# Kernel tuning notes

Hardware: AMD Instinct MI355X
Metric: run time of the kernel (lower is better)

## Reference

```python
import jax, jax.numpy as jnp
import numpy as np

H = 768      # hidden_size
NH = 12      # num_attention_heads
DH = H // NH # attention_head_size
FF = 3072    # intermediate_size
E = 4        # n_expert
B, S = 8, 512
EPS = 1e-12


def _layernorm(x, g, b):
    mu = jnp.mean(x, axis=-1, keepdims=True)
    var = jnp.var(x, axis=-1, keepdims=True)
    return (x - mu) * jax.lax.rsqrt(var + EPS) * g + b


def _expert_linear(x, W, b, expert_idx):
    # W: [E, in, out], b: [E, out]; gather per-sample expert weights, then batched GEMM.
    # Mathematically identical to running every expert then slicing (single_select_fwd).
    Wg = W[expert_idx]            # [B, in, out]
    bg = b[expert_idx]            # [B, out]
    return jnp.einsum('bsi,bio->bso', x, Wg) + bg[:, None, :]


def setup_inputs() -> dict:
    key = jax.random.key(0)
    ks = jax.random.split(key, 16)
    sc = 0.02
    inp = {
        'hidden_states': jax.random.normal(ks[0], (B, S, H), jnp.float32),
        'expert_idx': jax.random.randint(ks[1], (B,), 0, E, jnp.int64) if jax.config.read('jax_enable_x64') else jax.random.randint(ks[1], (B,), 0, E).astype(jnp.int32),
        'attention_mask': jnp.zeros((B, 1, 1, S), jnp.float32),
        'Wq': sc * jax.random.normal(ks[2], (E, H, H), jnp.float32),
        'bq': jnp.zeros((E, H), jnp.float32),
        'Wk': sc * jax.random.normal(ks[3], (E, H, H), jnp.float32),
        'bk': jnp.zeros((E, H), jnp.float32),
        'Wv': sc * jax.random.normal(ks[4], (E, H, H), jnp.float32),
        'bv': jnp.zeros((E, H), jnp.float32),
        'Wo': sc * jax.random.normal(ks[5], (E, H, H), jnp.float32),
        'bo': jnp.zeros((E, H), jnp.float32),
        'ln1_g': jnp.ones((H,), jnp.float32),
        'ln1_b': jnp.zeros((H,), jnp.float32),
        'Wi': sc * jax.random.normal(ks[6], (E, H, FF), jnp.float32),
        'bi': jnp.zeros((E, FF), jnp.float32),
        'Wout': sc * jax.random.normal(ks[7], (E, FF, H), jnp.float32),
        'bout': jnp.zeros((E, H), jnp.float32),
        'ln2_g': jnp.ones((H,), jnp.float32),
        'ln2_b': jnp.zeros((H,), jnp.float32),
    }
    return inp


def reference(hidden_states, expert_idx, attention_mask, Wq, bq, Wk, bk, Wv, bv,
              Wo, bo, ln1_g, ln1_b, Wi, bi, Wout, bout, ln2_g, ln2_b):
    b, s, h = hidden_states.shape
    # --- MoE self-attention (per-sample expert QKV) ---
    q = _expert_linear(hidden_states, Wq, bq, expert_idx).reshape(b, s, NH, DH).transpose(0, 2, 1, 3)
    k = _expert_linear(hidden_states, Wk, bk, expert_idx).reshape(b, s, NH, DH).transpose(0, 2, 1, 3)
    v = _expert_linear(hidden_states, Wv, bv, expert_idx).reshape(b, s, NH, DH).transpose(0, 2, 1, 3)
    scores = jnp.einsum('bhqd,bhkd->bhqk', q, k) / np.sqrt(DH).astype(np.float32)
    scores = scores + attention_mask
    probs = jax.nn.softmax(scores, axis=-1)
    ctx = jnp.einsum('bhqk,bhkd->bhqd', probs, v).transpose(0, 2, 1, 3).reshape(b, s, h)
    # --- MoE self-output: dense + residual + LN ---
    attn_out = _expert_linear(ctx, Wo, bo, expert_idx)
    x = _layernorm(attn_out + hidden_states, ln1_g, ln1_b)
    # --- MoE FFN: intermediate (GELU) + output + residual + LN ---
    hmid = jax.nn.gelu(_expert_linear(x, Wi, bi, expert_idx), approximate=False)
    ffn = _expert_linear(hmid, Wout, bout, expert_idx)
    return _layernorm(ffn + x, ln2_g, ln2_b)
```

## Files before the change

### kernel.cpp

```cpp
#include <hip/hip_runtime.h>
#include <cstdint>
#include <cstddef>

constexpr int CB  = 8;
constexpr int CS  = 512;
constexpr int CH  = 768;
constexpr int CNH = 12;
constexpr int CDH = 64;
constexpr int CFF = 3072;
constexpr int CE  = 4;
constexpr int C3H = 3 * CH;

using f32x4  = __attribute__((ext_vector_type(4))) float;
using bf16x8 = __attribute__((ext_vector_type(8))) short;

__device__ __forceinline__ short f2bf(float x) {
  union { float f; uint32_t u; } v; v.f = x;
  return (short)((v.u + 0x7fffu + ((v.u >> 16) & 1u)) >> 16);
}

__device__ __forceinline__ void gload_lds16(const void* g, void* l) {
  __builtin_amdgcn_global_load_lds((const __attribute__((address_space(1))) void*)g,
                                   (__attribute__((address_space(3))) void*)l,
                                   16, 0, 0);
}

#define VMCNT(n)  asm volatile("s_waitcnt vmcnt(" #n ")" ::: "memory")
#define SCHEDB()  __builtin_amdgcn_sched_barrier(0)

__global__ void cvt_bf16_kernel(const float* __restrict__ in, short* __restrict__ out, int n4) {
  int i = blockIdx.x * blockDim.x + threadIdx.x;
  if (i < n4) {
    float4 v = ((const float4*)in)[i];
    short4 o;
    o.x = f2bf(v.x); o.y = f2bf(v.y); o.z = f2bf(v.z); o.w = f2bf(v.w);
    ((short4*)out)[i] = o;
  }
}

__device__ __forceinline__ bool expert_used(const int* __restrict__ eidx, int e) {
  bool u = false;
#pragma unroll
  for (int s = 0; s < CB; ++s) u |= (eidx[s] == e);
  return u;
}

__device__ __forceinline__ void tpose_body(const float* __restrict__ Wb,
                                           short* __restrict__ Wtb, int K, int N) {
  __shared__ __align__(16) short Ts[64 * 68];
  const int n0 = blockIdx.x * 64, k0 = blockIdx.y * 64;
  const int t  = threadIdx.x;
  const int tn = t & 15, tk = t >> 4;
#pragma unroll
  for (int p = 0; p < 4; ++p) {
    int k = k0 + p * 16 + tk;
    float4 v = *(const float4*)(Wb + (size_t)k * N + n0 + tn * 4);
#pragma unroll
    for (int j = 0; j < 4; ++j)
      Ts[(tn * 4 + j) * 68 + p * 16 + tk] = f2bf(((const float*)&v)[j]);
  }
  __syncthreads();
#pragma unroll
  for (int p = 0; p < 4; ++p) {
    int n = n0 + p * 16 + tk;
    uint2 o = *(const uint2*)(Ts + (p * 16 + tk) * 68 + tn * 4);
    *(uint2*)(Wtb + (size_t)n * K + k0 + tn * 4) = o;
  }
}

__global__ void tpose_cvt_kernel(const float* __restrict__ W, short* __restrict__ Wt,
                                 const int* __restrict__ eidx, int K, int N) {
  const int e = blockIdx.z;
  if (!expert_used(eidx, e)) return;
  tpose_body(W + (size_t)e * K * N, Wt + (size_t)e * K * N, K, N);
}

__global__ void tpose4_kernel(const float* __restrict__ Wq, const float* __restrict__ Wk,
                              const float* __restrict__ Wv, const float* __restrict__ Wo,
                              const int* __restrict__ eidx,
                              short* __restrict__ Wqkvt, short* __restrict__ Wot) {
  const int z = blockIdx.z, e = z >> 2, m = z & 3;
  if (!expert_used(eidx, e)) return;
  const float* W = (m == 0) ? Wq : (m == 1) ? Wk : (m == 2) ? Wv : Wo;
  const float* Wb = W + (size_t)e * CH * CH;
  short* dst = (m == 3) ? (Wot + (size_t)e * CH * CH)
                        : (Wqkvt + ((size_t)e * C3H + m * CH) * CH);
  tpose_body(Wb, dst, CH, CH);
}

__global__ void qkv_bias_kernel(const float* __restrict__ bq, const float* __restrict__ bk,
                                const float* __restrict__ bv, float* __restrict__ dst) {
  int i = blockIdx.x * 256 + threadIdx.x;
  if (i >= CE * C3H) return;
  int e = i / C3H, r = i % C3H;
  int m = r / CH, c = r % CH;
  const float* s = (m == 0) ? bq : (m == 1) ? bk : bv;
  dst[i] = s[e * CH + c];
}

template <int BM, int NTN, int KSPLIT, int NJB, int NNB>
__device__ __forceinline__ void moe_decode(const int* __restrict__ eidx,
                                           int& e, int& mrow0, int& nt, int& ks) {
  constexpr int JC  = 4096 / BM;
  constexpr int MTS = CS / BM;
  constexpr int CHJ = JC / NJB;
  constexpr int CHN = NTN / NNB;
  constexpr int NKB = 8 / (NJB * NNB);
  constexpr int CHK = KSPLIT / NKB;
  int exv[CB];
#pragma unroll
  for (int s = 0; s < CB; ++s) exv[s] = eidx[s];
  uint32_t epack = 0;
#pragma unroll
  for (int s = 0; s < CB; ++s) epack |= (uint32_t)exv[s] << (2 * s);
  int c0 = 0, c1 = 0, c2 = 0;
#pragma unroll
  for (int s = 0; s < CB; ++s) {
    c0 += (exv[s] == 0); c1 += (exv[s] == 1); c2 += (exv[s] == 2);
  }
  int p0 = 0, p1 = c0, p2 = c0 + c1, p3 = c0 + c1 + c2;
  uint32_t sortedPack = 0;
#pragma unroll
  for (int s = 0; s < CB; ++s) {
    int ee = exv[s];
    int p = (ee == 0) ? p0 : (ee == 1) ? p1 : (ee == 2) ? p2 : p3;
    sortedPack |= (uint32_t)s << (4 * p);
    p0 += (ee == 0); p1 += (ee == 1); p2 += (ee == 2); p3 += (ee == 3);
  }
  const int x = (int)blockIdx.x & 7;
  const int i = (int)blockIdx.x >> 3;
  const int kb = x / (NJB * NNB);
  const int rx = x - kb * (NJB * NNB);
  const int jb = rx / NNB, nb = rx - (rx / NNB) * NNB;
  const int nn = i % CHN;
  const int rem = i / CHN;
  const int jj = rem % CHJ;
  const int kk2 = rem / CHJ;
  const int j = jb * CHJ + jj;
  nt = nb * CHN + nn;
  ks = kb * CHK + kk2;
  const int sample = (int)((sortedPack >> (4 * (j / MTS))) & 7);
  e = (int)((epack >> (2 * sample)) & 3);
  mrow0 = sample * CS + (j % MTS) * BM;
}

template <int K, int NTN, int KSPLIT, int NJB, int NNB, int ACT, bool OB16>
__global__ __launch_bounds__(256, 2)
void gemm7_kernel(const short* __restrict__ A, const short* __restrict__ Wt,
                  const float* __restrict__ bias, const int* __restrict__ eidx,
                  char* __restrict__ out, char* __restrict__ out2,
                  size_t wtExpStride, int biasStride, int outLd, size_t outKsStride) {
  constexpr int BM = 128, BN = 192;
  constexpr int MI = 4, NI = 6;
  constexpr int NT = K / KSPLIT / 64;
  __shared__ __align__(16) short As[2][BM * 64];
  __shared__ __align__(16) short Bs[2][BN * 64];
  const int t = threadIdx.x, w = t >> 6, l = t & 63, lr = l & 15, lg = l >> 4;

  int e, mrow0, nt, ks;
  moe_decode<BM, NTN, KSPLIT, NJB, NNB>(eidx, e, mrow0, nt, ks);
  const int kBase = ks * NT * 64;

  const int srow = t >> 3;
  const int gcol = (((t & 7) ^ ((t >> 3) & 7)) * 8);
  const short* aSrc = A + (size_t)(mrow0 + srow) * K + kBase + gcol;
  const short* bSrc = Wt + (size_t)e * wtExpStride + (size_t)(nt * BN + srow) * K + kBase + gcol;
  const size_t iss32 = (size_t)32 * K;

  const int wrow = (w >> 1) * 64, wn = (w & 1) * 96;
  int aoff[2][MI], boff[2][NI];
#pragma unroll
  for (int kk = 0; kk < 2; ++kk) {
    const int slot = (kk * 4 + lg) ^ (lr & 7);
#pragma unroll
    for (int mi = 0; mi < MI; ++mi)
      aoff[kk][mi] = (wrow + mi * 16 + lr) * 64 + slot * 8;
#pragma unroll
    for (int ni = 0; ni < NI; ++ni)
      boff[kk][ni] = (wn + ni * 16 + lr) * 64 + slot * 8;
  }

  f32x4 acc[MI][NI] = {};

  auto STAGE_A = [&](int buf, int kt) {
    const short* as = aSrc + (size_t)kt * 64;
#pragma unroll
    for (int i = 0; i < 4; ++i)
      gload_lds16(as + i * iss32, &As[buf][i * 2048 + t * 8]);
  };
  auto STAGE_B = [&](int buf, int kt) {
    const short* bs = bSrc + (size_t)kt * 64;
#pragma unroll
    for (int i = 0; i < 6; ++i)
      gload_lds16(bs + i * iss32, &Bs[buf][i * 2048 + t * 8]);
  };

  STAGE_A(0, 0);
  STAGE_B(0, 0);

  for (int kt = 0; kt < NT; ++kt) {
    const int buf = kt & 1;
    if (kt + 1 < NT) { STAGE_A(buf ^ 1, kt + 1); VMCNT(4); }
    else             { VMCNT(0); }
    __builtin_amdgcn_s_barrier();
    SCHEDB();
    {
      bf16x8 af[MI], bfr[NI];
#pragma unroll
      for (int ni = 0; ni < NI; ++ni) bfr[ni] = *(const bf16x8*)(&Bs[buf][boff[0][ni]]);
#pragma unroll
      for (int mi = 0; mi < MI; ++mi) af[mi] = *(const bf16x8*)(&As[buf][aoff[0][mi]]);
      __builtin_amdgcn_s_setprio(1);
#pragma unroll
      for (int mi = 0; mi < MI; ++mi)
#pragma unroll
        for (int ni = 0; ni < NI; ++ni)
          acc[mi][ni] = __builtin_amdgcn_mfma_f32_16x16x32_bf16(af[mi], bfr[ni],
                                                                acc[mi][ni], 0, 0, 0);
      __builtin_amdgcn_s_setprio(0);
    }
    if (kt + 1 < NT) STAGE_B(buf ^ 1, kt + 1);
    {
      bf16x8 af[MI], bfr[NI];
#pragma unroll
      for (int ni = 0; ni < NI; ++ni) bfr[ni] = *(const bf16x8*)(&Bs[buf][boff[1][ni]]);
#pragma unroll
      for (int mi = 0; mi < MI; ++mi) af[mi] = *(const bf16x8*)(&As[buf][aoff[1][mi]]);
      __builtin_amdgcn_s_setprio(1);
#pragma unroll
      for (int mi = 0; mi < MI; ++mi)
#pragma unroll
        for (int ni = 0; ni < NI; ++ni)
          acc[mi][ni] = __builtin_amdgcn_mfma_f32_16x16x32_bf16(af[mi], bfr[ni],
                                                                acc[mi][ni], 0, 0, 0);
      __builtin_amdgcn_s_setprio(0);
    }
    __builtin_amdgcn_s_barrier();
    SCHEDB();
  }

  float* outF = (ks < 2) ? ((float*)out + (size_t)ks * outKsStride)
                         : ((float*)out2 + (size_t)(ks - 2) * outKsStride);
#pragma unroll
  for (int ni = 0; ni < NI; ++ni) {
    const int col = nt * BN + wn + ni * 16 + lr;
    const float bv = bias ? bias[e * biasStride + col] : 0.0f;
#pragma unroll
    for (int mi = 0; mi < MI; ++mi) {
      const int row0 = mrow0 + wrow + mi * 16 + lg * 4;
#pragma unroll
      for (int r = 0; r < 4; ++r) {
        float v = acc[mi][ni][r] + bv;
        if (ACT == 1) v = 0.5f * v * (1.0f + erff(v * 0.70710678118654752f));
        if (OB16) ((short*)out)[(size_t)(row0 + r) * outLd + col] = f2bf(v);
        else      outF[(size_t)(row0 + r) * outLd + col] = v;
      }
    }
  }
}

__global__ void attn_kernel(const short* __restrict__ QKV, const float* __restrict__ mask,
                            short* __restrict__ ctx) {
  __shared__ __align__(16) short Vt[2][64 * 40];
  __shared__ __align__(16) short Pt[4][2][16 * 40];
  const int bh = blockIdx.x;
  const int b = bh / CNH, h = bh % CNH;
  const int qt = blockIdx.y;
  const int t = threadIdx.x, w = t >> 6, l = t & 63, lr = l & 15, lg = l >> 4;

  const size_t bS = (size_t)b * CS;
  const short* Qh = QKV + bS * C3H + h * CDH;
  const short* Kh = Qh + CH;
  const short* Vh = Qh + 2 * CH;
  const float* mrow = mask + bS;

  const int qrow = qt * 64 + w * 16 + lr;
  bf16x8 qa[2];
  qa[0] = *(const bf16x8*)(Qh + (size_t)qrow * C3H + lg * 8);
  qa[1] = *(const bf16x8*)(Qh + (size_t)qrow * C3H + 32 + lg * 8);

  f32x4 o[4] = {};
  float lp[4] = {0.f, 0.f, 0.f, 0.f};

  const int dh = t & 63, kg = t >> 6;
  {
    short v8[8];
#pragma unroll
    for (int j = 0; j < 8; ++j) v8[j] = Vh[(size_t)(kg * 8 + j) * C3H + dh];
    uint32_t p0 = (uint32_t)(uint16_t)v8[0] | ((uint32_t)(uint16_t)v8[1] << 16);
    uint32_t p1 = (uint32_t)(uint16_t)v8[2] | ((uint32_t)(uint16_t)v8[3] << 16);
    uint32_t p2 = (uint32_t)(uint16_t)v8[4] | ((uint32_t)(uint16_t)v8[5] << 16);
    uint32_t p3 = (uint32_t)(uint16_t)v8[6] | ((uint32_t)(uint16_t)v8[7] << 16);
    uint4 pk = {p0, p1, p2, p3};
    *(uint4*)(&Vt[0][dh * 40 + kg * 8]) = pk;
  }

  for (int tt = 0; tt < CS / 32; ++tt) {
    const int k0 = tt * 32;
    __syncthreads();

    f32x4 sacc[2] = {};
#pragma unroll
    for (int n = 0; n < 2; ++n) {
      bf16x8 kb0 = *(const bf16x8*)(Kh + (size_t)(k0 + n * 16 + lr) * C3H + lg * 8);
      bf16x8 kb1 = *(const bf16x8*)(Kh + (size_t)(k0 + n * 16 + lr) * C3H + 32 + lg * 8);
      sacc[n] = __builtin_amdgcn_mfma_f32_16x16x32_bf16(qa[0], kb0, sacc[n], 0, 0, 0);
      sacc[n] = __builtin_amdgcn_mfma_f32_16x16x32_bf16(qa[1], kb1, sacc[n], 0, 0, 0);
    }

    if (tt + 1 < CS / 32) {
      const int k1 = k0 + 32;
      short v8[8];
#pragma unroll
      for (int j = 0; j < 8; ++j) v8[j] = Vh[(size_t)(k1 + kg * 8 + j) * C3H + dh];
      uint32_t p0 = (uint32_t)(uint16_t)v8[0] | ((uint32_t)(uint16_t)v8[1] << 16);
      uint32_t p1 = (uint32_t)(uint16_t)v8[2] | ((uint32_t)(uint16_t)v8[3] << 16);
      uint32_t p2 = (uint32_t)(uint16_t)v8[4] | ((uint32_t)(uint16_t)v8[5] << 16);
      uint32_t p3 = (uint32_t)(uint16_t)v8[6] | ((uint32_t)(uint16_t)v8[7] << 16);
      uint4 pk = {p0, p1, p2, p3};
      *(uint4*)(&Vt[(tt + 1) & 1][dh * 40 + kg * 8]) = pk;
    }

    const int pb = tt & 1;
#pragma unroll
    for (int n = 0; n < 2; ++n) {
      float mv = mrow[k0 + n * 16 + lr];
#pragma unroll
      for (int r = 0; r < 4; ++r) {
        float s = sacc[n][r] * 0.125f + mv;
        float e = __expf(s);
        lp[r] += e;
        Pt[w][pb][(lg * 4 + r) * 40 + n * 16 + lr] = f2bf(e);
      }
    }

    bf16x8 pa = *(const bf16x8*)(&Pt[w][pb][lr * 40 + lg * 8]);
#pragma unroll
    for (int d = 0; d < 4; ++d) {
      bf16x8 vbf = *(const bf16x8*)(&Vt[tt & 1][(d * 16 + lr) * 40 + lg * 8]);
      o[d] = __builtin_amdgcn_mfma_f32_16x16x32_bf16(pa, vbf, o[d], 0, 0, 0);
    }
  }

#pragma unroll
  for (int r = 0; r < 4; ++r) {
    float s = lp[r];
    s += __shfl_xor(s, 1); s += __shfl_xor(s, 2);
    s += __shfl_xor(s, 4); s += __shfl_xor(s, 8);
    lp[r] = 1.0f / s;
  }
#pragma unroll
  for (int d = 0; d < 4; ++d)
#pragma unroll
    for (int r = 0; r < 4; ++r) {
      int row = qt * 64 + w * 16 + lg * 4 + r;
      ctx[(bS + row) * CH + h * CDH + d * 16 + lr] = f2bf(o[d][r] * lp[r]);
    }
}

template <int NP>
__global__ void ln12_kernel(const float* __restrict__ p0, const float* __restrict__ p1,
                            const float* __restrict__ p2, const float* __restrict__ p3,
                            const float* __restrict__ res,
                            const float* __restrict__ btab, const int* __restrict__ eidx,
                            const float* __restrict__ g, const float* __restrict__ bta,
                            float* __restrict__ out32, short* __restrict__ out16) {
  const int row = blockIdx.x;
  const int l = threadIdx.x;
  const int e = eidx[row >> 9];
  const float* xr0 = p0 + (size_t)row * CH;
  const float* xr1 = p1 + (size_t)row * CH;
  const float* rr  = res + (size_t)row * CH;
  const float* bo  = btab + (size_t)e * CH;
  float4 v[3];
  float sum = 0.f, ss = 0.f;
#pragma unroll
  for (int j = 0; j < 3; ++j) {
    float4 a = *(const float4*)(xr0 + j * 256 + l * 4);
    float4 c = *(const float4*)(xr1 + j * 256 + l * 4);
    float4 b = *(const float4*)(rr + j * 256 + l * 4);
    float4 bb = *(const float4*)(bo + j * 256 + l * 4);
    a.x += c.x + b.x + bb.x; a.y += c.y + b.y + bb.y;
    a.z += c.z + b.z + bb.z; a.w += c.w + b.w + bb.w;
    if (NP == 4) {
      float4 d2 = *(const float4*)(p2 + (size_t)row * CH + j * 256 + l * 4);
      float4 d3 = *(const float4*)(p3 + (size_t)row * CH + j * 256 + l * 4);
      a.x += d2.x + d3.x; a.y += d2.y + d3.y;
      a.z += d2.z + d3.z; a.w += d2.w + d3.w;
    }
    v[j] = a;
    sum += a.x + a.y + a.z + a.w;
    ss  += a.x * a.x + a.y * a.y + a.z * a.z + a.w * a.w;
  }
#pragma unroll
  for (int m = 1; m < 64; m <<= 1) { sum += __shfl_xor(sum, m); ss += __shfl_xor(ss, m); }
  const float mean = sum * (1.0f / CH);
  const float var  = ss * (1.0f / CH) - mean * mean;
  const float rstd = rsqrtf(var + 1e-12f);
#pragma unroll
  for (int j = 0; j < 3; ++j) {
    float4 gg = *(const float4*)(g   + j * 256 + l * 4);
    float4 bb = *(const float4*)(bta + j * 256 + l * 4);
    float4 a = v[j], y;
    y.x = (a.x - mean) * rstd * gg.x + bb.x;
    y.y = (a.y - mean) * rstd * gg.y + bb.y;
    y.z = (a.z - mean) * rstd * gg.z + bb.z;
    y.w = (a.w - mean) * rstd * gg.w + bb.w;
    *(float4*)(out32 + (size_t)row * CH + j * 256 + l * 4) = y;
    if (out16) {
      short4 o;
      o.x = f2bf(y.x); o.y = f2bf(y.y); o.z = f2bf(y.z); o.w = f2bf(y.w);
      *(short4*)(out16 + (size_t)row * CH + j * 256 + l * 4) = o;
    }
  }
}

extern "C" void kernel_launch(void* const* d_in, const int* in_sizes, int n_in,
                              void* d_out, int out_size, void* d_ws, size_t ws_size,
                              hipStream_t stream) {
  (void)in_sizes; (void)n_in; (void)out_size; (void)ws_size;
  const float* hidden = (const float*)d_in[0];
  const int*   eidx   = (const int*)d_in[1];
  const float* mask   = (const float*)d_in[2];
  const float* Wq   = (const float*)d_in[3];
  const float* bq   = (const float*)d_in[4];
  const float* Wk   = (const float*)d_in[5];
  const float* bk   = (const float*)d_in[6];
  const float* Wv   = (const float*)d_in[7];
  const float* bv   = (const float*)d_in[8];
  const float* Wo   = (const float*)d_in[9];
  const float* bo   = (const float*)d_in[10];
  const float* ln1g = (const float*)d_in[11];
  const float* ln1b = (const float*)d_in[12];
  const float* Wi   = (const float*)d_in[13];
  const float* bi   = (const float*)d_in[14];
  const float* Wout = (const float*)d_in[15];
  const float* bout = (const float*)d_in[16];
  const float* ln2g = (const float*)d_in[17];
  const float* ln2b = (const float*)d_in[18];

  char* ws = (char*)d_ws;
  size_t off = 0;
  auto alloc = [&](size_t bytes) {
    void* p = ws + off;
    off += (bytes + 255) & ~(size_t)255;
    return p;
  };
  const size_t M = (size_t)CB * CS;
  short* Xb    = (short*)alloc(M * CH * 2);
  char*  Rbig  = (char*)alloc(M * CFF * 2);
  char*  Rcx   = (char*)alloc(M * CH * 4);
  float* parts = (float*)alloc(2 * M * CH * 4);
  float* qkvbias = (float*)alloc(CE * C3H * 4);
  short* Wqkvt = (short*)alloc((size_t)CE * C3H * CH * 2);
  short* Wot   = (short*)alloc((size_t)CE * CH * CH * 2);
  short* Wit   = (short*)alloc((size_t)CE * CH * CFF * 2);
  short* Wo2t  = (short*)alloc((size_t)CE * CFF * CH * 2);
  short* QKVb = (short*)Rbig;
  short* hmid = (short*)Rbig;
  short* ctxb = (short*)Rcx;
  float* x1   = (float*)Rcx;
  short* x1b  = Xb;
  float* pp2  = (float*)Wqkvt;
  float* pp3  = pp2 + M * CH;

  const int n4 = (int)(M * CH / 4);
  cvt_bf16_kernel<<<(n4 + 255) / 256, 256, 0, stream>>>(hidden, Xb, n4);
  tpose4_kernel<<<dim3(CH / 64, CH / 64, 4 * CE), 256, 0, stream>>>(Wq, Wk, Wv, Wo, eidx, Wqkvt, Wot);
  tpose_cvt_kernel<<<dim3(CFF / 64, CH / 64, CE), 256, 0, stream>>>(Wi, Wit, eidx, CH, CFF);
  tpose_cvt_kernel<<<dim3(CH / 64, CFF / 64, CE), 256, 0, stream>>>(Wout, Wo2t, eidx, CFF, CH);
  qkv_bias_kernel<<<(CE * C3H + 255) / 256, 256, 0, stream>>>(bq, bk, bv, qkvbias);

  gemm7_kernel<CH, 12, 1, 4, 2, 0, true><<<384, 256, 0, stream>>>(
      Xb, Wqkvt, qkvbias, eidx, (char*)QKVb, nullptr, (size_t)C3H * CH, C3H, C3H, 0);
  attn_kernel<<<dim3(CB * CNH, CS / 64), 256, 0, stream>>>(QKVb, mask, ctxb);
  gemm7_kernel<CH, 4, 2, 4, 1, 0, false><<<256, 256, 0, stream>>>(
      ctxb, Wot, nullptr, eidx, (char*)parts, nullptr, (size_t)CH * CH, CH, CH, M * CH);
  ln12_kernel<2><<<(int)M, 64, 0, stream>>>(parts, parts + M * CH, nullptr, nullptr,
                                            hidden, bo, eidx, ln1g, ln1b, x1, x1b);
  gemm7_kernel<CH, 16, 1, 4, 2, 1, true><<<512, 256, 0, stream>>>(
      x1b, Wit, bi, eidx, (char*)hmid, nullptr, (size_t)CH * CFF, CFF, CFF, 0);
  gemm7_kernel<CFF, 4, 4, 2, 1, 0, false><<<512, 256, 0, stream>>>(
      hmid, Wo2t, nullptr, eidx, (char*)parts, (char*)pp2, (size_t)CFF * CH, CH, CH, M * CH);
  ln12_kernel<4><<<(int)M, 64, 0, stream>>>(parts, parts + M * CH, pp2, pp3,
                                            x1, bout, eidx, ln2g, ln2b, (float*)d_out, nullptr);
}
```

Before: 189.0 us.

## Replace double-buffered BK=64 GEMM pipeline with single-buffered BK=128 tiles

The GEMM kernel switches from a double-buffered LDS pipeline with 64-wide K tiles to a single buffer holding 128-wide K tiles. It loads the whole tile, waits for all loads, then runs four MFMA sub-steps, with a matching 16-slot XOR swizzle. This halves the number of barriers and loop iterations, but loads are no longer overlapped with compute inside a block. It relies on the two co-resident blocks per CU to hide memory latency. Shared memory per block stays the same size.

```diff
diff --git a/kernel.cpp b/kernel.cpp
--- a/kernel.cpp
+++ b/kernel.cpp
@@ -146,86 +146,63 @@
 
 template <int K, int NTN, int KSPLIT, int NJB, int NNB, int ACT, bool OB16>
 __global__ __launch_bounds__(256, 2)
-void gemm7_kernel(const short* __restrict__ A, const short* __restrict__ Wt,
+void gemm8_kernel(const short* __restrict__ A, const short* __restrict__ Wt,
                   const float* __restrict__ bias, const int* __restrict__ eidx,
                   char* __restrict__ out, char* __restrict__ out2,
                   size_t wtExpStride, int biasStride, int outLd, size_t outKsStride) {
   constexpr int BM = 128, BN = 192;
   constexpr int MI = 4, NI = 6;
-  constexpr int NT = K / KSPLIT / 64;
-  __shared__ __align__(16) short As[2][BM * 64];
-  __shared__ __align__(16) short Bs[2][BN * 64];
+  constexpr int NT = K / KSPLIT / 128;
+  __shared__ __align__(16) short As[BM * 128];
+  __shared__ __align__(16) short Bs[BN * 128];
   const int t = threadIdx.x, w = t >> 6, l = t & 63, lr = l & 15, lg = l >> 4;
 
   int e, mrow0, nt, ks;
   moe_decode<BM, NTN, KSPLIT, NJB, NNB>(eidx, e, mrow0, nt, ks);
-  const int kBase = ks * NT * 64;
-
-  const int srow = t >> 3;
-  const int gcol = (((t & 7) ^ ((t >> 3) & 7)) * 8);
+  const int kBase = ks * NT * 128;
+
+  const int srow = t >> 4;
+  const int gcol = ((t & 15) ^ srow) * 8;
   const short* aSrc = A + (size_t)(mrow0 + srow) * K + kBase + gcol;
   const short* bSrc = Wt + (size_t)e * wtExpStride + (size_t)(nt * BN + srow) * K + kBase + gcol;
-  const size_t iss32 = (size_t)32 * K;
+  const size_t iss16 = (size_t)16 * K;
 
   const int wrow = (w >> 1) * 64, wn = (w & 1) * 96;
-  int aoff[2][MI], boff[2][NI];
-#pragma unroll
-  for (int kk = 0; kk < 2; ++kk) {
-    const int slot = (kk * 4 + lg) ^ (lr & 7);
+  int aoff[4][MI], boff[4][NI];
+#pragma unroll
+  for (int kk = 0; kk < 4; ++kk) {
+    const int c = (kk * 4 + lg) ^ lr;
 #pragma unroll
     for (int mi = 0; mi < MI; ++mi)
-      aoff[kk][mi] = (wrow + mi * 16 + lr) * 64 + slot * 8;
+      aoff[kk][mi] = (wrow + mi * 16 + lr) * 128 + c * 8;
 #pragma unroll
     for (int ni = 0; ni < NI; ++ni)
-      boff[kk][ni] = (wn + ni * 16 + lr) * 64 + slot * 8;
+      boff[kk][ni] = (wn + ni * 16 + lr) * 128 + c * 8;
   }
 
   f32x4 acc[MI][NI] = {};
 
-  auto STAGE_A = [&](int buf, int kt) {
-    const short* as = aSrc + (size_t)kt * 64;
-#pragma unroll
-    for (int i = 0; i < 4; ++i)
-      gload_lds16(as + i * iss32, &As[buf][i * 2048 + t * 8]);
-  };
-  auto STAGE_B = [&](int buf, int kt) {
-    const short* bs = bSrc + (size_t)kt * 64;
-#pragma unroll
-    for (int i = 0; i < 6; ++i)
-      gload_lds16(bs + i * iss32, &Bs[buf][i * 2048 + t * 8]);
-  };
-
-  STAGE_A(0, 0);
-  STAGE_B(0, 0);
-
   for (int kt = 0; kt < NT; ++kt) {
-    const int buf = kt & 1;
-    if (kt + 1 < NT) { STAGE_A(buf ^ 1, kt + 1); VMCNT(4); }
-    else             { VMCNT(0); }
+    {
+      const short* as = aSrc + (size_t)kt * 128;
+#pragma unroll
+      for (int i = 0; i < 8; ++i)
+        gload_lds16(as + i * iss16, &As[i * 2048 + t * 8]);
+      const short* bs = bSrc + (size_t)kt * 128;
+#pragma unroll
+      for (int i = 0; i < 12; ++i)
+        gload_lds16(bs + i * iss16, &Bs[i * 2048 + t * 8]);
+    }
+    VMCNT(0);
     __builtin_amdgcn_s_barrier();
     SCHEDB();
-    {
+#pragma unroll
+    for (int kk = 0; kk < 4; ++kk) {
       bf16x8 af[MI], bfr[NI];
 #pragma unroll
-      for (int ni = 0; ni < NI; ++ni) bfr[ni] = *(const bf16x8*)(&Bs[buf][boff[0][ni]]);
-#pragma unroll
-      for (int mi = 0; mi < MI; ++mi) af[mi] = *(const bf16x8*)(&As[buf][aoff[0][mi]]);
-      __builtin_amdgcn_s_setprio(1);
-#pragma unroll
-      for (int mi = 0; mi < MI; ++mi)
-#pragma unroll
-        for (int ni = 0; ni < NI; ++ni)
-          acc[mi][ni] = __builtin_amdgcn_mfma_f32_16x16x32_bf16(af[mi], bfr[ni],
-                                                                acc[mi][ni], 0, 0, 0);
-      __builtin_amdgcn_s_setprio(0);
-    }
-    if (kt + 1 < NT) STAGE_B(buf ^ 1, kt + 1);
-    {
-      bf16x8 af[MI], bfr[NI];
-#pragma unroll
-      for (int ni = 0; ni < NI; ++ni) bfr[ni] = *(const bf16x8*)(&Bs[buf][boff[1][ni]]);
-#pragma unroll
-      for (int mi = 0; mi < MI; ++mi) af[mi] = *(const bf16x8*)(&As[buf][aoff[1][mi]]);
+      for (int ni = 0; ni < NI; ++ni) bfr[ni] = *(const bf16x8*)(&Bs[boff[kk][ni]]);
+#pragma unroll
+      for (int mi = 0; mi < MI; ++mi) af[mi] = *(const bf16x8*)(&As[aoff[kk][mi]]);
       __builtin_amdgcn_s_setprio(1);
 #pragma unroll
       for (int mi = 0; mi < MI; ++mi)
@@ -471,16 +448,16 @@
   tpose_cvt_kernel<<<dim3(CH / 64, CFF / 64, CE), 256, 0, stream>>>(Wout, Wo2t, eidx, CFF, CH);
   qkv_bias_kernel<<<(CE * C3H + 255) / 256, 256, 0, stream>>>(bq, bk, bv, qkvbias);
 
-  gemm7_kernel<CH, 12, 1, 4, 2, 0, true><<<384, 256, 0, stream>>>(
+  gemm8_kernel<CH, 12, 1, 4, 2, 0, true><<<384, 256, 0, stream>>>(
       Xb, Wqkvt, qkvbias, eidx, (char*)QKVb, nullptr, (size_t)C3H * CH, C3H, C3H, 0);
   attn_kernel<<<dim3(CB * CNH, CS / 64), 256, 0, stream>>>(QKVb, mask, ctxb);
-  gemm7_kernel<CH, 4, 2, 4, 1, 0, false><<<256, 256, 0, stream>>>(
+  gemm8_kernel<CH, 4, 2, 4, 1, 0, false><<<256, 256, 0, stream>>>(
       ctxb, Wot, nullptr, eidx, (char*)parts, nullptr, (size_t)CH * CH, CH, CH, M * CH);
   ln12_kernel<2><<<(int)M, 64, 0, stream>>>(parts, parts + M * CH, nullptr, nullptr,
                                             hidden, bo, eidx, ln1g, ln1b, x1, x1b);
-  gemm7_kernel<CH, 16, 1, 4, 2, 1, true><<<512, 256, 0, stream>>>(
+  gemm8_kernel<CH, 16, 1, 4, 2, 1, true><<<512, 256, 0, stream>>>(
       x1b, Wit, bi, eidx, (char*)hmid, nullptr, (size_t)CH * CFF, CFF, CFF, 0);
-  gemm7_kernel<CFF, 4, 4, 2, 1, 0, false><<<512, 256, 0, stream>>>(
+  gemm8_kernel<CFF, 4, 4, 2, 1, 0, false><<<512, 256, 0, stream>>>(
       hmid, Wo2t, nullptr, eidx, (char*)parts, (char*)pp2, (size_t)CFF * CH, CH, CH, M * CH);
   ln12_kernel<4><<<(int)M, 64, 0, stream>>>(parts, parts + M * CH, pp2, pp3,
                                             x1, bout, eidx, ln2g, ln2b, (float*)d_out, nullptr);
```

Measured after the change: 186.5 us. Within noise of the previous version (-1.4%).
